# Kernel optimization log

Measured on AMD Instinct MI355X. Metric: run time of the kernel, lower is better.

The kernel has to match this reference:

```python
import jax, jax.numpy as jnp
import numpy as np

N = 100000   # num nodes
E = 1600000  # num edges
D = 64       # feature / hidden dim (irreps_in == hidden_dim)
SCALE = D ** -0.5


def setup_inputs() -> dict:
    key = jax.random.key(0)
    ks = jax.random.split(key, 6)
    x = jax.random.normal(ks[0], (N, D), dtype=jnp.float32)
    edge_index = jax.random.randint(ks[1], (2, E), 0, N, dtype=jnp.int32)
    std = D ** -0.5
    Wq = jax.random.normal(ks[2], (D, D), dtype=jnp.float32) * std
    Wk = jax.random.normal(ks[3], (D, D), dtype=jnp.float32) * std
    Wv = jax.random.normal(ks[4], (D, D), dtype=jnp.float32) * std
    Wo = jax.random.normal(ks[5], (D, D), dtype=jnp.float32) * std
    return {"x": x, "edge_index": edge_index, "Wq": Wq, "Wk": Wk, "Wv": Wv, "Wo": Wo}


def reference(x, edge_index, Wq, Wk, Wv, Wo):
    # Per-receiver variable-length attention over incoming neighbors.
    # Mathematically identical to the torch module's degree-bucketed SDPA
    # (softmax over each node's neighbor set), without padding buffers.
    sender, receiver = edge_index[0], edge_index[1]
    Q = x @ Wq  # [N, D]
    K = x @ Wk
    V = x @ Wv
    # per-edge logits: <Q[receiver], K[sender]> * scale
    s = jnp.einsum('ed,ed->e', Q[receiver], K[sender]) * SCALE  # [E]
    # numerically stable segment softmax over receiver groups
    m = jax.ops.segment_max(s, receiver, num_segments=N)  # -inf for empty segments
    m_safe = jnp.where(jnp.isfinite(m), m, 0.0)
    p = jnp.exp(s - m_safe[receiver])  # [E]
    denom = jax.ops.segment_sum(p, receiver, num_segments=N)  # [N]
    num = jax.ops.segment_sum(p[:, None] * V[sender], receiver, num_segments=N)  # [N, D]
    # zero-degree nodes get out = 0 (matches torch: skipped buckets + nan_to_num)
    out = jnp.where(denom[:, None] > 0,
                    num / jnp.maximum(denom, 1e-30)[:, None],
                    0.0)
    return x + out @ Wo
```

## Files before the change

### kernel.cpp

```cpp
#include <hip/hip_runtime.h>
#include <hip/hip_bf16.h>

#define DIM 64
#define SCALE 0.125f
#define BINSH 5
#define NPB 32
#define BCAP 768
#define DBSH 8
#define NDB 256
#define CBCAP 4864
#define CHUNKA 16384
#define MAXCB 512

static __device__ __forceinline__ unsigned int pack2bf(float a, float b) {
    unsigned int ua = __float_as_uint(a), ub = __float_as_uint(b);
    ua += 0x7fffu + ((ua >> 16) & 1u);
    ub += 0x7fffu + ((ub >> 16) & 1u);
    return (ua >> 16) | (ub & 0xffff0000u);
}
static __device__ __forceinline__ float2 unpack2bf(unsigned int u) {
    return make_float2(__uint_as_float(u << 16), __uint_as_float(u & 0xffff0000u));
}

__global__ __launch_bounds__(1024) void k_prepA(const int* __restrict__ send,
                                                const int* __restrict__ recv,
                                                const float* __restrict__ Wv,
                                                const float* __restrict__ Wo,
                                                float* __restrict__ Wvo,
                                                int* __restrict__ bucketCur,
                                                unsigned int* __restrict__ cbuf,
                                                int E, int NCB) {
    __shared__ __align__(16) float smem[8192];
    int* hist = (int*)smem;
    int* lcur = hist + MAXCB;
    int tid = threadIdx.x;

    if (blockIdx.x == 0) {
        float* av = smem;
        float* bo = smem + 4096;
        ((float4*)av)[tid] = ((const float4*)Wv)[tid];
        ((float4*)bo)[tid] = ((const float4*)Wo)[tid];
        __syncthreads();
        int r = tid >> 4, c0 = (tid & 15) * 4;
        float acc[4] = {0.f, 0.f, 0.f, 0.f};
        for (int k = 0; k < 64; k++) {
            float a = av[r * 64 + k];
#pragma unroll
            for (int j = 0; j < 4; j++) acc[j] = fmaf(a, bo[k * 64 + c0 + j], acc[j]);
        }
#pragma unroll
        for (int j = 0; j < 4; j++) Wvo[r * 64 + c0 + j] = acc[j];
        __syncthreads();
    }

    int base = blockIdx.x * CHUNKA;
    int lim = min(base + CHUNKA, E);

    for (int i = tid; i < NCB; i += 1024) hist[i] = 0;
    __syncthreads();
    for (int i = base + tid; i < lim; i += 1024)
        atomicAdd(&hist[recv[i] >> DBSH], 1);
    __syncthreads();
    for (int i = tid; i < NCB; i += 1024) {
        int h = hist[i];
        lcur[i] = h ? atomicAdd(&bucketCur[i], h) : 0;
    }
    __syncthreads();
    for (int i = base + tid; i < lim; i += 1024) {
        int r = recv[i];
        int b = r >> DBSH;
        int p = atomicAdd(&lcur[b], 1);
        if (p < CBCAP)
            cbuf[(size_t)b * CBCAP + p] =
                (unsigned)send[i] | ((unsigned)(r & (NDB - 1)) << 17);
    }
}

__global__ __launch_bounds__(256) void k_fused(const float* __restrict__ x,
                                               const float* __restrict__ Wq,
                                               const float* __restrict__ Wk,
                                               const float* __restrict__ Wvo,
                                               const int* __restrict__ bucketCur,
                                               unsigned int* __restrict__ cbuf,
                                               int* __restrict__ nstart,
                                               int* __restrict__ ncount,
                                               float* __restrict__ Q,
                                               unsigned int* __restrict__ KVb,
                                               int N, int NCB, int nchunk) {
    __shared__ __align__(16) float smem[8192];
    int tid = threadIdx.x;
    int wv = tid >> 6;
    int lane = tid & 63;

    if ((int)blockIdx.x < NCB) {
        int b = blockIdx.x;
        int bbase = b * CBCAP;
        int cnt = min(bucketCur[b], CBCAP);
        unsigned int* elist = (unsigned int*)smem;
        int* ldeg = (int*)smem + CBCAP;
        int* lcur = ldeg + NDB;
        int* wsum = lcur + NDB;

        for (int i = tid; i < cnt; i += 256) elist[i] = cbuf[bbase + i];
        ldeg[tid] = 0;
        __syncthreads();
        for (int i = tid; i < cnt; i += 256)
            atomicAdd(&ldeg[(elist[i] >> 17) & (NDB - 1)], 1);
        __syncthreads();

        int d = ldeg[tid];
        int incl = d;
        for (int o = 1; o < 64; o <<= 1) {
            int t = __shfl_up(incl, o, 64);
            if (lane >= o) incl += t;
        }
        if (lane == 63) wsum[wv] = incl;
        __syncthreads();
        int woff = 0;
        for (int w2 = 0; w2 < wv; w2++) woff += wsum[w2];
        int start = woff + incl - d;
        lcur[tid] = start;
        int r = (b << DBSH) + tid;
        if (r < N) {
            nstart[r] = bbase + start;
            ncount[r] = d;
        }
        __syncthreads();

        for (int i = tid; i < cnt; i += 256) {
            unsigned u = elist[i];
            int n = (u >> 17) & (NDB - 1);
            int p = atomicAdd(&lcur[n], 1);
            cbuf[bbase + p] = u & 0x1FFFFu;
        }
        return;
    }

    int qb = blockIdx.x - NCB;
    int m = qb / nchunk;
    int cb = qb % nchunk;
    const float* W = (m == 0) ? Wq : ((m == 1) ? Wk : Wvo);

    int base = cb * 256 + wv * 64;
    if (base < N) {
        float* xw = smem + wv * 2048;
        int lr = lane >> 3;
        int lc = lane & 7;
        const float* xp = xw + lr * 8;

        float acc[8][8];
#pragma unroll
        for (int i = 0; i < 8; i++)
#pragma unroll
            for (int j = 0; j < 8; j++) acc[i][j] = 0.f;

#pragma unroll
        for (int h = 0; h < 2; h++) {
#pragma unroll
            for (int c4 = 0; c4 < 8; c4++) {
                float4 v = make_float4(0.f, 0.f, 0.f, 0.f);
                if (base + lane < N)
                    v = ((const float4*)x)[(size_t)(base + lane) * 16 + h * 8 + c4];
                xw[(c4 * 4 + 0) * 64 + lane] = v.x;
                xw[(c4 * 4 + 1) * 64 + lane] = v.y;
                xw[(c4 * 4 + 2) * 64 + lane] = v.z;
                xw[(c4 * 4 + 3) * 64 + lane] = v.w;
            }
            asm volatile("s_waitcnt lgkmcnt(0)" ::: "memory");

            const float* wp = W + h * 2048 + lc * 8;

            float4 xa = *(const float4*)(xp);
            float4 xb = *(const float4*)(xp + 4);
            float4 wa0 = *(const float4*)(wp);
            float4 wb0 = *(const float4*)(wp + 4);
            float4 wa1 = *(const float4*)(wp + 64);
            float4 wb1 = *(const float4*)(wp + 68);
#pragma unroll 4
            for (int kk = 0; kk < 32; kk++) {
                float4 xan, xbn, wan, wbn;
                if (kk < 31) {
                    xan = *(const float4*)(xp + (kk + 1) * 64);
                    xbn = *(const float4*)(xp + (kk + 1) * 64 + 4);
                }
                if (kk < 30) {
                    wan = *(const float4*)(wp + (kk + 2) * 64);
                    wbn = *(const float4*)(wp + (kk + 2) * 64 + 4);
                }
                float xv[8] = {xa.x, xa.y, xa.z, xa.w, xb.x, xb.y, xb.z, xb.w};
                float wc[8] = {wa0.x, wa0.y, wa0.z, wa0.w, wb0.x, wb0.y, wb0.z, wb0.w};
#pragma unroll
                for (int i = 0; i < 8; i++)
#pragma unroll
                    for (int j = 0; j < 8; j++)
                        acc[i][j] = fmaf(xv[i], wc[j], acc[i][j]);
                xa = xan; xb = xbn;
                wa0 = wa1; wb0 = wb1;
                wa1 = wan; wb1 = wbn;
            }
        }

#pragma unroll
        for (int i = 0; i < 8; i++) {
            int row = base + lr * 8 + i;
            if (row < N) {
                if (m == 0) {
                    float* dst = &Q[(size_t)row * 64 + lc * 8];
                    ((float4*)dst)[0] = make_float4(acc[i][0], acc[i][1], acc[i][2], acc[i][3]);
                    ((float4*)dst)[1] = make_float4(acc[i][4], acc[i][5], acc[i][6], acc[i][7]);
                } else {
                    unsigned int* dst = &KVb[(size_t)row * 64 + (m - 1) * 32 + lc * 4];
                    uint4 pk;
                    pk.x = pack2bf(acc[i][0], acc[i][1]);
                    pk.y = pack2bf(acc[i][2], acc[i][3]);
                    pk.z = pack2bf(acc[i][4], acc[i][5]);
                    pk.w = pack2bf(acc[i][6], acc[i][7]);
                    *((uint4*)dst) = pk;
                }
            }
        }
    }
}

__global__ __launch_bounds__(256) void k_attn(const float* __restrict__ Q,
                                              const unsigned int* __restrict__ KVb,
                                              const float* __restrict__ x,
                                              const int* __restrict__ nstart,
                                              const int* __restrict__ ncount,
                                              const unsigned int* __restrict__ nlist,
                                              float* __restrict__ out, int N) {
    __shared__ unsigned int llist[BCAP];
    __shared__ int lofs[NPB + 1];
    __shared__ int sbs;
    int tid = threadIdx.x;
    int wv = tid >> 6;
    int lane = tid & 63;
    int g = lane >> 3;
    int sub = lane & 7;

    int j = blockIdx.x;
    int r0 = j << BINSH;

    if (tid == 0) sbs = nstart[r0];
    __syncthreads();
    int sbase = sbs;
    if (tid < NPB) {
        int r = r0 + tid;
        lofs[tid] = min(nstart[r] - sbase, BCAP);
        if (tid == NPB - 1)
            lofs[NPB] = min(nstart[r] + ncount[r] - sbase, BCAP);
    }
    __syncthreads();
    int cnt = lofs[NPB];
    for (int i = tid; i < cnt; i += 256) llist[i] = nlist[sbase + i];
    __syncthreads();

    for (int n = wv; n < NPB; n += 4) {
        int r = r0 + n;
        if (r >= N) break;
        int start = lofs[n];
        int end = lofs[n + 1];
        float4 qa = *((const float4*)&Q[(size_t)r * 64 + sub * 8]);
        float4 qb = *((const float4*)&Q[(size_t)r * 64 + sub * 8 + 4]);
        float q[8] = {qa.x, qa.y, qa.z, qa.w, qb.x, qb.y, qb.z, qb.w};
        float acc[8] = {0.f, 0.f, 0.f, 0.f, 0.f, 0.f, 0.f, 0.f};
        float dpart = 0.f;

        int eA = start + g;
        bool vA = eA < end;
        unsigned int sA = vA ? llist[eA] : 0u;
        uint4 kA = *((const uint4*)&KVb[(size_t)sA * 64 + sub * 4]);
        uint4 uA = *((const uint4*)&KVb[(size_t)sA * 64 + 32 + sub * 4]);
        int eB = start + 8 + g;
        bool vB = eB < end;
        unsigned int sB = vB ? llist[eB] : 0u;
        uint4 kB = *((const uint4*)&KVb[(size_t)sB * 64 + sub * 4]);
        uint4 uB = *((const uint4*)&KVb[(size_t)sB * 64 + 32 + sub * 4]);

        for (int bb = start; bb < end; bb += 8) {
            int eC = bb + 16 + g;
            bool vC = eC < end;
            unsigned int sC = vC ? llist[eC] : 0u;
            uint4 kC = *((const uint4*)&KVb[(size_t)sC * 64 + sub * 4]);
            uint4 uC = *((const uint4*)&KVb[(size_t)sC * 64 + 32 + sub * 4]);

            float2 k01 = unpack2bf(kA.x), k23 = unpack2bf(kA.y);
            float2 k45 = unpack2bf(kA.z), k67 = unpack2bf(kA.w);
            float dot = q[0] * k01.x + q[1] * k01.y + q[2] * k23.x + q[3] * k23.y
                      + q[4] * k45.x + q[5] * k45.y + q[6] * k67.x + q[7] * k67.y;
            dot += __shfl_xor(dot, 1);
            dot += __shfl_xor(dot, 2);
            dot += __shfl_xor(dot, 4);
            float w = vA ? __expf(dot * SCALE) : 0.f;

            float2 v01 = unpack2bf(uA.x), v23 = unpack2bf(uA.y);
            float2 v45 = unpack2bf(uA.z), v67 = unpack2bf(uA.w);
            acc[0] = fmaf(w, v01.x, acc[0]);
            acc[1] = fmaf(w, v01.y, acc[1]);
            acc[2] = fmaf(w, v23.x, acc[2]);
            acc[3] = fmaf(w, v23.y, acc[3]);
            acc[4] = fmaf(w, v45.x, acc[4]);
            acc[5] = fmaf(w, v45.y, acc[5]);
            acc[6] = fmaf(w, v67.x, acc[6]);
            acc[7] = fmaf(w, v67.y, acc[7]);
            dpart += w;

            kA = kB; uA = uB; vA = vB;
            kB = kC; uB = uC; vB = vC;
        }

        dpart += __shfl_xor(dpart, 8); dpart += __shfl_xor(dpart, 16); dpart += __shfl_xor(dpart, 32);
#pragma unroll
        for (int jj = 0; jj < 8; jj++) {
            acc[jj] += __shfl_xor(acc[jj], 8);
            acc[jj] += __shfl_xor(acc[jj], 16);
            acc[jj] += __shfl_xor(acc[jj], 32);
        }

        float inv = (dpart > 0.f) ? (1.0f / dpart) : 0.f;

        if (g == 0) {
            float4 xa = *((const float4*)&x[(size_t)r * 64 + sub * 8]);
            float4 xb = *((const float4*)&x[(size_t)r * 64 + sub * 8 + 4]);
            float4 oa = make_float4(fmaf(acc[0], inv, xa.x), fmaf(acc[1], inv, xa.y),
                                    fmaf(acc[2], inv, xa.z), fmaf(acc[3], inv, xa.w));
            float4 ob = make_float4(fmaf(acc[4], inv, xb.x), fmaf(acc[5], inv, xb.y),
                                    fmaf(acc[6], inv, xb.z), fmaf(acc[7], inv, xb.w));
            *((float4*)&out[(size_t)r * 64 + sub * 8]) = oa;
            *((float4*)&out[(size_t)r * 64 + sub * 8 + 4]) = ob;
        }
    }
}


extern "C" void kernel_launch(void* const* d_in, const int* in_sizes, int n_in,
                              void* d_out, int out_size, void* d_ws, size_t ws_size,
                              hipStream_t stream) {
    const float* x  = (const float*)d_in[0];
    const int* edge = (const int*)d_in[1];
    const float* Wq = (const float*)d_in[2];
    const float* Wk = (const float*)d_in[3];
    const float* Wv = (const float*)d_in[4];
    const float* Wo = (const float*)d_in[5];
    float* out = (float*)d_out;

    int N = in_sizes[0] / DIM;
    int E = in_sizes[1] / 2;
    int NBK = (N + NPB - 1) >> BINSH;
    int NCB = (N + NDB - 1) >> DBSH;

    char* p = (char*)d_ws;
    auto cv = [&](size_t bytes) {
        char* r = p;
        p += ((bytes + 255) / 256) * 256;
        return r;
    };
    float*        Q         = (float*)cv((size_t)N * 64 * 4);
    unsigned int* KVb       = (unsigned int*)cv((size_t)N * 64 * 4);
    float*        Wvo       = (float*)cv(64 * 64 * 4);
    int*          bucketCur = (int*)cv((size_t)NCB * 4);
    unsigned int* cbuf      = (unsigned int*)cv((size_t)NCB * CBCAP * 4);
    int*          nstart    = (int*)cv((size_t)N * 4);
    int*          ncount    = (int*)cv((size_t)N * 4);
    (void)ws_size; (void)n_in; (void)out_size;

    const int* send = edge;
    const int* recv = edge + E;

    int NBA = (E + CHUNKA - 1) / CHUNKA;
    int nchunk = (N + 255) / 256;

    hipMemsetAsync(bucketCur, 0, (size_t)NCB * 4, stream);
    k_prepA<<<NBA, 1024, 0, stream>>>(send, recv, Wv, Wo, Wvo, bucketCur, cbuf, E, NCB);
    k_fused<<<NCB + 3 * nchunk, 256, 0, stream>>>(x, Wq, Wk, Wvo, bucketCur, cbuf,
                                                  nstart, ncount, Q, KVb,
                                                  N, NCB, nchunk);
    k_attn<<<NBK, 256, 0, stream>>>(Q, KVb, x, nstart, ncount, cbuf, out, N);
}
```

Baseline: 236.4 us.

## Stage bucketed edges in shared memory for coalesced global scatter

```diff
diff --git a/kernel.cpp b/kernel.cpp
--- a/kernel.cpp
+++ b/kernel.cpp
@@ -9,7 +9,7 @@
 #define DBSH 8
 #define NDB 256
 #define CBCAP 4864
-#define CHUNKA 16384
+#define CHUNKA 8192
 #define MAXCB 512
 
 static __device__ __forceinline__ unsigned int pack2bf(float a, float b) {
@@ -30,14 +30,18 @@
                                                 int* __restrict__ bucketCur,
                                                 unsigned int* __restrict__ cbuf,
                                                 int E, int NCB) {
-    __shared__ __align__(16) float smem[8192];
-    int* hist = (int*)smem;
-    int* lcur = hist + MAXCB;
+    __shared__ __align__(16) unsigned int elist[CHUNKA];
+    __shared__ int hist[MAXCB];
+    __shared__ int lofs[MAXCB + 1];
+    __shared__ int gbase[MAXCB];
+    __shared__ int lcur[MAXCB];
+    __shared__ int wsum[8];
     int tid = threadIdx.x;
+    int lane = tid & 63;
 
     if (blockIdx.x == 0) {
-        float* av = smem;
-        float* bo = smem + 4096;
+        float* av = (float*)elist;
+        float* bo = (float*)elist + 4096;
         ((float4*)av)[tid] = ((const float4*)Wv)[tid];
         ((float4*)bo)[tid] = ((const float4*)Wo)[tid];
         __syncthreads();
@@ -55,24 +59,56 @@
 
     int base = blockIdx.x * CHUNKA;
     int lim = min(base + CHUNKA, E);
+    int cnt = lim - base;
 
     for (int i = tid; i < NCB; i += 1024) hist[i] = 0;
     __syncthreads();
     for (int i = base + tid; i < lim; i += 1024)
         atomicAdd(&hist[recv[i] >> DBSH], 1);
     __syncthreads();
-    for (int i = tid; i < NCB; i += 1024) {
-        int h = hist[i];
-        lcur[i] = h ? atomicAdd(&bucketCur[i], h) : 0;
-    }
-    __syncthreads();
+
+    {
+        int d = (tid < NCB) ? hist[tid] : 0;
+        int incl = d;
+        for (int o = 1; o < 64; o <<= 1) {
+            int t2 = __shfl_up(incl, o, 64);
+            if (lane >= o) incl += t2;
+        }
+        if (tid < 512 && lane == 63) wsum[tid >> 6] = incl;
+        __syncthreads();
+        if (tid == 0) {
+            int a = 0;
+#pragma unroll
+            for (int i2 = 0; i2 < 8; i2++) { int v = wsum[i2]; wsum[i2] = a; a += v; }
+        }
+        __syncthreads();
+        if (tid < NCB) {
+            int excl = incl - d + wsum[tid >> 6];
+            lofs[tid] = excl;
+            lcur[tid] = excl;
+            gbase[tid] = d ? atomicAdd(&bucketCur[tid], d) : 0;
+        }
+        if (tid == 0) lofs[NCB] = cnt;
+    }
+    __syncthreads();
+
     for (int i = base + tid; i < lim; i += 1024) {
         int r = recv[i];
         int b = r >> DBSH;
         int p = atomicAdd(&lcur[b], 1);
-        if (p < CBCAP)
-            cbuf[(size_t)b * CBCAP + p] =
-                (unsigned)send[i] | ((unsigned)(r & (NDB - 1)) << 17);
+        elist[p] = (unsigned)send[i] | ((unsigned)(r & (NDB - 1)) << 17);
+    }
+    __syncthreads();
+
+    for (int i = tid; i < cnt; i += 1024) {
+        int lo = 0, hi = NCB;
+        while (hi - lo > 1) {
+            int mid = (lo + hi) >> 1;
+            if (lofs[mid] <= i) lo = mid; else hi = mid;
+        }
+        int pos = gbase[lo] + (i - lofs[lo]);
+        if (pos < CBCAP)
+            cbuf[(size_t)lo * CBCAP + pos] = elist[i];
     }
 }
 
```

After: 230.8 us. 2.4% less time.
